# Kernel tuning notes

Hardware: AMD Instinct MI355X
Metric: run time of the kernel (lower is better)

The kernel has to match this reference:

```python
import jax, jax.numpy as jnp
import numpy as np
from jax import lax

B, C, L = 2048, 9605, 8
WL_PER_LABEL = 50
ALPHA = 0.5        # training_config['alpha4']
ALPHA1 = 0.1       # margin
ALPHA2 = 2.0       # training_config['alpha2']
ALPHA3 = 10.0      # training_config['alpha3']
ALPHA_OTHER = 0.5
NEG = jnp.float32(-1e30)


def setup_inputs() -> dict:
    key = jax.random.key(0)
    k1, k2, k3, k4 = jax.random.split(key, 4)
    x = jax.random.normal(k1, (B, C), dtype=jnp.float32) * 2.0
    y = (jax.random.uniform(k2, (B, C)) < 0.005).astype(jnp.float32)
    y_neg = (jax.random.uniform(k3, (B, C)) < 0.005).astype(jnp.float32)
    # whitelist masks: L app-labels, each whitelisting ~WL_PER_LABEL raw classes
    idx = jax.random.randint(k4, (L, WL_PER_LABEL), 0, C)
    wl_masks = jnp.zeros((L, C), dtype=bool).at[jnp.arange(L)[:, None], idx].set(True)
    return {"x": x, "y": y, "y_neg": y_neg, "wl_masks": wl_masks}


def reference(x, y, y_neg, wl_masks):
    # y_neg is consumed by the original forward (find_gt_whitelist) but never
    # affects the returned loss, faithfully ignored here.
    xs_pos = jax.nn.sigmoid(x)                                  # [B, C]
    # top_k_thres = max(11th-largest sigmoid, alpha_other)
    thres = jnp.maximum(lax.top_k(xs_pos, 11)[0][:, 10], ALPHA_OTHER)  # [B]
    # per-label whitelist max: m[b,l] = max_{c in wl_l} xs_pos[b,c]
    m = jnp.max(jnp.where(wl_masks[None, :, :], xs_pos[:, None, :], NEG), axis=-1)  # [B, L]
    # label l is a ground-truth whitelist label iff y has any positive in wl_l
    has_pos = jnp.einsum('bc,lc->bl', y, wl_masks.astype(y.dtype)) > 0   # [B, L]
    correct_max = jnp.max(jnp.where(has_pos, m, NEG), axis=-1)           # [B]
    incorrect_max = jnp.max(jnp.where(~has_pos, m, NEG), axis=-1)        # [B]
    any_correct = jnp.any(has_pos, axis=-1)
    any_incorrect = jnp.any(~has_pos, axis=-1)
    # union whitelist max (the "other" branch uses xs_pos over all wl indices)
    union_max = jnp.max(jnp.where(jnp.any(wl_masks, axis=0)[None, :], xs_pos, NEG), axis=-1)
    x1 = jnp.where(any_correct, correct_max, thres)
    x2 = jnp.where(any_correct,
                   jnp.where(any_incorrect, jnp.maximum(incorrect_max, thres), thres),
                   union_max)
    coef = jnp.where(any_correct, 1.0, 1.0 - ALPHA)
    d = x2 - x1 + ALPHA1
    rank = jnp.where(d > 0, ALPHA2, 1.0) * jax.nn.sigmoid(ALPHA3 * d)
    return jnp.mean(coef * rank)
```

## Files before the change

### kernel.cpp

```cpp
#include <hip/hip_runtime.h>

#define CC 9605
#define BB 2048
#define LL 8
#define NEGF (-1e30f)
#define NINF (-__builtin_huge_valf())

#define WS_PARTIALS_OFF 16384

__device__ __forceinline__ unsigned enc_f(float f) {
  unsigned u = __float_as_uint(f);
  return (u & 0x80000000u) ? ~u : (u | 0x80000000u);
}
__device__ __forceinline__ float dec_u(unsigned e) {
  unsigned u = (e & 0x80000000u) ? (e & 0x7fffffffu) : ~e;
  return __uint_as_float(u);
}
__device__ __forceinline__ float sigm(float z) {
  return 1.0f / (1.0f + __expf(-z));
}

__global__ void wl_sniff(const unsigned* __restrict__ wlw,
                         unsigned* __restrict__ wsu) {
  const int nwords = (LL * CC) / 4;
  const int stride = gridDim.x * blockDim.x;
  unsigned f = 0u;
  for (int j = blockIdx.x * blockDim.x + threadIdx.x; j < nwords; j += stride) {
    unsigned w = wlw[j];
#pragma unroll
    for (int k = 0; k < 4; ++k) {
      unsigned b = (w >> (8 * k)) & 255u;
      if (b == 1u)    { f |= 2u; if (k != 0) f |= 1u; }
      if (b == 0x3fu) { f |= 8u; if (k == 1) f |= 4u; }
    }
  }
#pragma unroll
  for (int off = 32; off >= 1; off >>= 1) f |= __shfl_xor(f, off, 64);
  if ((threadIdx.x & 63) == 0 && f) atomicOr(&wsu[1], f);
}

__global__ void wl_compact(const unsigned char* __restrict__ wl,
                           unsigned* __restrict__ wsu) {
  const int tid = threadIdx.x;
  const int lane = tid & 63;
  const int c = blockIdx.x * 256 + tid;
  const unsigned g = wsu[1];
  const int dt = (g & 1u) ? 0 : (g & 4u) ? 3 : (g & 2u) ? 1 : (g & 8u) ? 2 : 0;
  const int* wl32 = (const int*)wl;
  const float* wlf = (const float*)wl;
  const unsigned short* wlh = (const unsigned short*)wl;
  unsigned m = 0u;
  if (c < CC) {
#pragma unroll
    for (int l = 0; l < LL; ++l) {
      int j = l * CC + c;
      bool on;
      if (dt == 0) on = (wl[j] != 0);
      else if (dt == 1) on = (wl32[j] != 0);
      else if (dt == 2) on = (wlf[j] != 0.0f);
      else on = (wlh[j] != 0);
      if (on) m |= (1u << l);
    }
  }
  unsigned long long bal = __ballot(m != 0u);
  if (bal) {
    unsigned wcnt = (unsigned)__popcll(bal);
    unsigned basep = 0u;
    if (lane == 0) basep = atomicAdd(&wsu[0], wcnt);
    basep = __shfl(basep, 0, 64);
    if (m) {
      unsigned pos = basep + (unsigned)__popcll(bal & ((1ull << lane) - 1ull));
      if (pos < 2048u) wsu[4 + pos] = ((unsigned)c << 8) | m;
    }
  }
}


#define FOR11(OP) OP(0) OP(1) OP(2) OP(3) OP(4) OP(5) OP(6) OP(7) OP(8) OP(9) OP(10)
#define FOR11I(OP) OP(0) OP(1) OP(2) OP(3) OP(4) OP(5) OP(6) OP(7) OP(8) OP(9) OP(10)
#define FOR8(OP) OP(0) OP(1) OP(2) OP(3) OP(4) OP(5) OP(6) OP(7)

#define DECL_S(k) float s_##k = NINF;
#define INS1(k) { float _hi = fmaxf(s_##k, cv); cv = fminf(s_##k, cv); s_##k = _hi; }
#define TOP11V(v) { float cv = (v); FOR11I(INS1) }
#define TOP4(T) { TOP11V((T).x) TOP11V((T).y) TOP11V((T).z) TOP11V((T).w) }

__global__ __launch_bounds__(256) void loss_kernel(
    const float* __restrict__ x, const float* __restrict__ y,
    const unsigned* __restrict__ wsu, float* __restrict__ partials) {
  __shared__ float sh_top[3][64][11];
  __shared__ float sh_wlm[4][8];
  __shared__ unsigned sh_wpm[4];

  const int tid = threadIdx.x;
  const int lane = tid & 63;
  const int w = tid >> 6;
  const int r = blockIdx.x;
  const long long base = (long long)r * CC;

  const unsigned nu = min(wsu[0], 2048u);
  const unsigned* ents = wsu + 4;

  const int soff = (4 - (r & 3)) & 3;
  const int ng = (CC - soff) >> 2;
  const int tailn = CC - soff - (ng << 2);
  const int m_extra = soff + tailn;
  const float4* vp = (const float4*)(x + base + soff);

  FOR11(DECL_S)

  const int g0 = 600 * w + lane;
#pragma unroll
  for (int k = 0; k < 9; ++k) {
    float4 t = vp[g0 + 64 * k];
    TOP4(t)
  }
  {
    float4 t = make_float4(NINF, NINF, NINF, NINF);
    if (lane < 24) t = vp[600 * w + 576 + lane];
    TOP4(t)
  }
  if (w == 3) {
    {
      float4 t = make_float4(NINF, NINF, NINF, NINF);
      if (2400 + lane < ng) t = vp[2400 + lane];
      TOP4(t)
    }
    float tv = NINF;
    if (lane < m_extra) {
      int tc = (lane < soff) ? lane : (soff + (ng << 2) + (lane - soff));
      tv = x[base + tc];
    }
    TOP11V(tv)
  }

  unsigned en0 = ((unsigned)tid < nu) ? ents[tid] : 0u;
  unsigned en1 = ((unsigned)tid + 256u < nu) ? ents[tid + 256] : 0u;
  float gx0 = x[base + (en0 >> 8)], gy0 = y[base + (en0 >> 8)];
  float gx1 = x[base + (en1 >> 8)], gy1 = y[base + (en1 >> 8)];

#define DECL_LM(k) float lm_##k = NEGF;
  FOR8(DECL_LM)
  unsigned pmask = 0u;
#define FOLDE(EN, GX, GY)                                        \
  {                                                              \
    unsigned mk = (EN) & 255u;    \
    pmask |= mk;                                                 \
    if ((GY) > 0.0f) pmask |= (mk << 8);                         \
    if (mk & 1u)   lm_0 = fmaxf(lm_0, (GX));                     \
    if (mk & 2u)   lm_1 = fmaxf(lm_1, (GX));                     \
    if (mk & 4u)   lm_2 = fmaxf(lm_2, (GX));                     \
    if (mk & 8u)   lm_3 = fmaxf(lm_3, (GX));                     \
    if (mk & 16u)  lm_4 = fmaxf(lm_4, (GX));                     \
    if (mk & 32u)  lm_5 = fmaxf(lm_5, (GX));                     \
    if (mk & 64u)  lm_6 = fmaxf(lm_6, (GX));                     \
    if (mk & 128u) lm_7 = fmaxf(lm_7, (GX));                     \
  }
  FOLDE(en0, gx0, gy0)
  FOLDE(en1, gx1, gy1)
  for (unsigned e = 512u + (unsigned)tid; e < nu; e += 256u) {
    unsigned ent = ents[e];
    float xv = x[base + (ent >> 8)];
    float yv = y[base + (ent >> 8)];
    FOLDE(ent, xv, yv)
  }
#pragma unroll
  for (int off = 32; off >= 1; off >>= 1) {
    pmask |= __shfl_xor(pmask, off, 64);
#define RED1(l) lm_##l = fmaxf(lm_##l, __shfl_xor(lm_##l, off, 64));
    FOR8(RED1)
#undef RED1
  }

  if (w > 0) {
#define ST1(k) sh_top[w - 1][lane][k] = s_##k;
    FOR11(ST1)
#undef ST1
  }
  if (lane == 0) {
#define STL(l) sh_wlm[w][l] = lm_##l;
    FOR8(STL)
#undef STL
    sh_wpm[w] = pmask;
  }
  __syncthreads();
  if (w != 0) return;

#pragma unroll
  for (int j = 0; j < 3; ++j) {
#pragma unroll
    for (int k = 0; k < 11; ++k) {
      TOP11V(sh_top[j][lane][k])
    }
  }

#define DECL_E(k) unsigned e_##k = enc_f(s_##k);
  FOR11(DECL_E)
#undef DECL_E
  unsigned wlo = e_10;
  unsigned whi = e_0;
#pragma unroll
  for (int off = 32; off >= 1; off >>= 1) {
    wlo = max(wlo, __shfl_xor(wlo, off, 64));
    whi = max(whi, __shfl_xor(whi, off, 64));
  }
  unsigned lo = wlo, hi = whi + 1u;
  while (hi - lo > 1u) {
    unsigned mid = lo + ((hi - lo) >> 1);
    unsigned cnt = 0u;
#define CMP1(k) cnt += (e_##k >= mid) ? 1u : 0u;
    FOR11(CMP1)
#undef CMP1
    unsigned tot = (unsigned)__popcll(__ballot(cnt & 1u)) +
                   ((unsigned)__popcll(__ballot(cnt & 2u)) << 1) +
                   ((unsigned)__popcll(__ballot(cnt & 4u)) << 2) +
                   ((unsigned)__popcll(__ballot(cnt & 8u)) << 3);
    if (tot >= 11u) lo = mid; else hi = mid;
  }
  const unsigned E11 = lo;

  if (lane == 0) {
#pragma unroll
    for (int j = 1; j < 4; ++j) {
      pmask |= sh_wpm[j];
#define CMB(l) lm_##l = fmaxf(lm_##l, sh_wlm[j][l]);
      FOR8(CMB)
#undef CMB
    }
    unsigned PR = pmask & 255u, PO = (pmask >> 8) & 255u;
    float thres = fmaxf(sigm(dec_u(E11)), 0.5f);
    float cmax = NEGF, imax = NEGF, umax = NEGF;
#define EP1(l)                                                   \
    if ((PR >> l) & 1u) {                                        \
      float ml = sigm(lm_##l);                                   \
      umax = fmaxf(umax, ml);                                    \
      if ((PO >> l) & 1u) cmax = fmaxf(cmax, ml);                \
      else imax = fmaxf(imax, ml);                               \
    }
    FOR8(EP1)
#undef EP1
    bool anyc = (PO != 0u);
    bool anyi = (PO != 255u);
    float x1 = anyc ? cmax : thres;
    float x2 = anyc ? (anyi ? fmaxf(imax, thres) : thres)
                    : ((nu > 0u) ? umax : NEGF);
    float coef = anyc ? 1.0f : 0.5f;
    float dd = x2 - x1 + 0.1f;
    float rank = ((dd > 0.0f) ? 2.0f : 1.0f) * sigm(10.0f * dd);
    partials[r] = coef * rank;
  }
}

__global__ void final_reduce(const float* __restrict__ partials,
                             float* __restrict__ out) {
  __shared__ float sh[4];
  const int tid = threadIdx.x;
  const int lane = tid & 63;
  const int wid = tid >> 6;
  float s = 0.0f;
  for (int i = tid; i < BB; i += 256) s += partials[i];
#pragma unroll
  for (int off = 32; off >= 1; off >>= 1) s += __shfl_xor(s, off, 64);
  if (lane == 0) sh[wid] = s;
  __syncthreads();
  if (tid == 0) out[0] = (sh[0] + sh[1] + sh[2] + sh[3]) * (1.0f / (float)BB);
}

extern "C" void kernel_launch(void* const* d_in, const int* in_sizes, int n_in,
                              void* d_out, int out_size, void* d_ws,
                              size_t ws_size, hipStream_t stream) {
  const float* x = (const float*)d_in[0];
  const float* y = (const float*)d_in[1];
  const unsigned char* wl = (const unsigned char*)d_in[3];
  float* out = (float*)d_out;
  unsigned* wsu = (unsigned*)d_ws;
  float* partials = (float*)((char*)d_ws + WS_PARTIALS_OFF);

  hipMemsetAsync(d_ws, 0, 16, stream);
  wl_sniff<<<64, 256, 0, stream>>>((const unsigned*)wl, wsu);
  wl_compact<<<(CC + 255) / 256, 256, 0, stream>>>(wl, wsu);
  loss_kernel<<<BB, 256, 0, stream>>>(x, y, wsu, partials);
  final_reduce<<<1, 256, 0, stream>>>(partials, out);
}
```

Baseline: 222.2 us.

## Replace per-thread top-11 insertion with rowmax-guided threshold compaction

```diff
diff --git a/kernel.cpp b/kernel.cpp
--- a/kernel.cpp
+++ b/kernel.cpp
@@ -3,10 +3,13 @@
 #define CC 9605
 #define BB 2048
 #define LL 8
+#define CAND_MAX 384
 #define NEGF (-1e30f)
 #define NINF (-__builtin_huge_valf())
+#define LOMIN 0x00800000u
 
 #define WS_PARTIALS_OFF 16384
+#define WS_ROWMAX_OFF 24576
 
 __device__ __forceinline__ unsigned enc_f(float f) {
   unsigned u = __float_as_uint(f);
@@ -75,76 +78,166 @@
   }
 }
 
-
-#define FOR11(OP) OP(0) OP(1) OP(2) OP(3) OP(4) OP(5) OP(6) OP(7) OP(8) OP(9) OP(10)
-#define FOR11I(OP) OP(0) OP(1) OP(2) OP(3) OP(4) OP(5) OP(6) OP(7) OP(8) OP(9) OP(10)
-#define FOR8(OP) OP(0) OP(1) OP(2) OP(3) OP(4) OP(5) OP(6) OP(7)
-
-#define DECL_S(k) float s_##k = NINF;
-#define INS1(k) { float _hi = fmaxf(s_##k, cv); cv = fminf(s_##k, cv); s_##k = _hi; }
-#define TOP11V(v) { float cv = (v); FOR11I(INS1) }
-#define TOP4(T) { TOP11V((T).x) TOP11V((T).y) TOP11V((T).z) TOP11V((T).w) }
-
-__global__ __launch_bounds__(256) void loss_kernel(
-    const float* __restrict__ x, const float* __restrict__ y,
-    const unsigned* __restrict__ wsu, float* __restrict__ partials) {
-  __shared__ float sh_top[3][64][11];
-  __shared__ float sh_wlm[4][8];
-  __shared__ unsigned sh_wpm[4];
-
-  const int tid = threadIdx.x;
-  const int lane = tid & 63;
-  const int w = tid >> 6;
+__global__ __launch_bounds__(256) void rowmax_kernel(
+    const float* __restrict__ x, unsigned* __restrict__ rowmax) {
+  __shared__ float shm[4];
+  const int tid = threadIdx.x, lane = tid & 63, wid = tid >> 6;
   const int r = blockIdx.x;
   const long long base = (long long)r * CC;
-
-  const unsigned nu = min(wsu[0], 2048u);
-  const unsigned* ents = wsu + 4;
-
   const int soff = (4 - (r & 3)) & 3;
   const int ng = (CC - soff) >> 2;
   const int tailn = CC - soff - (ng << 2);
   const int m_extra = soff + tailn;
   const float4* vp = (const float4*)(x + base + soff);
-
-  FOR11(DECL_S)
-
-  const int g0 = 600 * w + lane;
+  float m = NINF;
 #pragma unroll
   for (int k = 0; k < 9; ++k) {
-    float4 t = vp[g0 + 64 * k];
-    TOP4(t)
+    float4 t = vp[tid + (k << 8)];
+    m = fmaxf(m, fmaxf(fmaxf(t.x, t.y), fmaxf(t.z, t.w)));
   }
   {
-    float4 t = make_float4(NINF, NINF, NINF, NINF);
-    if (lane < 24) t = vp[600 * w + 576 + lane];
-    TOP4(t)
-  }
-  if (w == 3) {
-    {
-      float4 t = make_float4(NINF, NINF, NINF, NINF);
-      if (2400 + lane < ng) t = vp[2400 + lane];
-      TOP4(t)
-    }
-    float tv = NINF;
-    if (lane < m_extra) {
-      int tc = (lane < soff) ? lane : (soff + (ng << 2) + (lane - soff));
-      tv = x[base + tc];
-    }
-    TOP11V(tv)
-  }
+    int gi = tid + 2304;
+    if (gi < ng) {
+      float4 t = vp[gi];
+      m = fmaxf(m, fmaxf(fmaxf(t.x, t.y), fmaxf(t.z, t.w)));
+    }
+  }
+  if (tid < m_extra) {
+    int tc = (tid < soff) ? tid : (soff + (ng << 2) + (tid - soff));
+    m = fmaxf(m, x[base + tc]);
+  }
+#pragma unroll
+  for (int off = 32; off >= 1; off >>= 1) m = fmaxf(m, __shfl_xor(m, off, 64));
+  if (lane == 0) shm[wid] = m;
+  __syncthreads();
+  if (tid == 0)
+    rowmax[r] = enc_f(fmaxf(fmaxf(shm[0], shm[1]), fmaxf(shm[2], shm[3])));
+}
+
+
+#define FOR8(OP) OP(0) OP(1) OP(2) OP(3) OP(4) OP(5) OP(6) OP(7)
+
+#define APPEND1(V, PRED)                                                     \
+  {                                                                          \
+    bool _p = (PRED);                                                        \
+    unsigned long long _bal = __ballot(_p);                                  \
+    if (_bal) {                                                              \
+      unsigned _wt = (unsigned)__popcll(_bal);                               \
+      unsigned _bp = 0u;                                                     \
+      if (lane == 0) _bp = atomicAdd(&sh_cnt, _wt);                          \
+      _bp = __shfl(_bp, 0, 64);                                              \
+      if (_p) {                                                              \
+        unsigned _pos =                                                      \
+            _bp + (unsigned)__popcll(_bal & ((1ull << lane) - 1ull));        \
+        if (_pos < CAND_MAX) sh_cand[_pos] = enc_f(V);                       \
+      }                                                                      \
+    }                                                                        \
+  }
+
+#define COMPACT_PASS(TENC, RES)                                              \
+  do {                                                                       \
+    float Tf = dec_u(TENC);                                                  \
+    __syncthreads();                                                         \
+    if (tid == 0) sh_cnt = 0u;                                               \
+    __syncthreads();                                                         \
+    _Pragma("unroll") for (int k = 0; k < 9; ++k) {                          \
+      float4 t = vp[tid + (k << 8)];                                         \
+      APPEND1(t.x, t.x >= Tf) APPEND1(t.y, t.y >= Tf)                        \
+      APPEND1(t.z, t.z >= Tf) APPEND1(t.w, t.w >= Tf)                        \
+    }                                                                        \
+    {                                                                        \
+      float4 t = make_float4(NINF, NINF, NINF, NINF);                        \
+      if (tid + 2304 < ng) t = vp[tid + 2304];                               \
+      APPEND1(t.x, t.x >= Tf) APPEND1(t.y, t.y >= Tf)                        \
+      APPEND1(t.z, t.z >= Tf) APPEND1(t.w, t.w >= Tf)                        \
+    }                                                                        \
+    APPEND1(tailv, tailv >= Tf)                                              \
+    __syncthreads();                                                         \
+    RES = sh_cnt;                                                            \
+  } while (0)
+
+#define COUNT_PASS(TENC, RES)                                                \
+  do {                                                                       \
+    float Tf = dec_u(TENC);                                                  \
+    unsigned cl = 0u;                                                        \
+    _Pragma("unroll") for (int k = 0; k < 9; ++k) {                          \
+      float4 t = vp[tid + (k << 8)];                                         \
+      cl += (t.x >= Tf) + (t.y >= Tf) + (t.z >= Tf) + (t.w >= Tf);           \
+    }                                                                        \
+    {                                                                        \
+      float4 t = make_float4(NINF, NINF, NINF, NINF);                        \
+      if (tid + 2304 < ng) t = vp[tid + 2304];                               \
+      cl += (t.x >= Tf) + (t.y >= Tf) + (t.z >= Tf) + (t.w >= Tf);           \
+    }                                                                        \
+    cl += (tailv >= Tf) ? 1u : 0u;                                           \
+    _Pragma("unroll") for (int off = 32; off >= 1; off >>= 1)                \
+        cl += __shfl_xor(cl, off, 64);                                       \
+    __syncthreads();                                                         \
+    if (lane == 0) sh_redC[wid] = cl;                                        \
+    __syncthreads();                                                         \
+    RES = sh_redC[0] + sh_redC[1] + sh_redC[2] + sh_redC[3];                 \
+  } while (0)
+
+__global__ __launch_bounds__(256) void loss_kernel(
+    const float* __restrict__ x, const float* __restrict__ y,
+    const unsigned* __restrict__ wsu, const unsigned* __restrict__ rowmax,
+    float* __restrict__ partials) {
+  __shared__ unsigned sh_cand[CAND_MAX];
+  __shared__ unsigned sh_redC[4];
+  __shared__ unsigned sh_cnt;
+  __shared__ float sh_wlm[4][8];
+  __shared__ unsigned sh_wpm[4];
+
+  const int tid = threadIdx.x, lane = tid & 63, wid = tid >> 6;
+  const int r = blockIdx.x;
+  const long long base = (long long)r * CC;
+  const int soff = (4 - (r & 3)) & 3;
+  const int ng = (CC - soff) >> 2;
+  const int tailn = CC - soff - (ng << 2);
+  const int m_extra = soff + tailn;
+  const float4* vp = (const float4*)(x + base + soff);
+  float tailv = NINF;
+  if (tid < m_extra) {
+    int tc = (tid < soff) ? tid : (soff + (ng << 2) + (tid - soff));
+    tailv = x[base + tc];
+  }
+  const unsigned Emax = rowmax[r];
+  const unsigned nu = min(wsu[0], 2048u);
+  const unsigned* ents = wsu + 4;
+
+  unsigned lo = (Emax > LOMIN + (1u << 22)) ? Emax - (1u << 22) : LOMIN;
+  unsigned hi = Emax + 1u;
+  unsigned c;
+  bool done = false;
+  unsigned E11 = 0u;
+  COMPACT_PASS(lo, c);
+  unsigned compLo = lo;
+  while (c < 11u && lo > LOMIN) {
+    hi = lo;
+    lo = (lo > LOMIN + (1u << 23)) ? lo - (1u << 23) : LOMIN;
+    COMPACT_PASS(lo, c);
+    compLo = lo;
+  }
+  if (c < 11u) { E11 = LOMIN; done = true; }
+  while (!done && c > CAND_MAX) {
+    if (hi - lo <= 1u) { E11 = lo; done = true; break; }
+    unsigned mid = lo + ((hi - lo) >> 1);
+    unsigned cm;
+    COUNT_PASS(mid, cm);
+    if (cm >= 11u) { lo = mid; c = cm; } else { hi = mid; }
+  }
+  if (!done && lo != compLo) { COMPACT_PASS(lo, c); }
 
   unsigned en0 = ((unsigned)tid < nu) ? ents[tid] : 0u;
   unsigned en1 = ((unsigned)tid + 256u < nu) ? ents[tid + 256] : 0u;
   float gx0 = x[base + (en0 >> 8)], gy0 = y[base + (en0 >> 8)];
   float gx1 = x[base + (en1 >> 8)], gy1 = y[base + (en1 >> 8)];
-
 #define DECL_LM(k) float lm_##k = NEGF;
   FOR8(DECL_LM)
   unsigned pmask = 0u;
 #define FOLDE(EN, GX, GY)                                        \
   {                                                              \
-    unsigned mk = (EN) & 255u;    \
+    unsigned mk = (EN) & 255u;                                   \
     pmask |= mk;                                                 \
     if ((GY) > 0.0f) pmask |= (mk << 8);                         \
     if (mk & 1u)   lm_0 = fmaxf(lm_0, (GX));                     \
@@ -171,53 +264,35 @@
     FOR8(RED1)
 #undef RED1
   }
-
-  if (w > 0) {
-#define ST1(k) sh_top[w - 1][lane][k] = s_##k;
-    FOR11(ST1)
-#undef ST1
-  }
   if (lane == 0) {
-#define STL(l) sh_wlm[w][l] = lm_##l;
+#define STL(l) sh_wlm[wid][l] = lm_##l;
     FOR8(STL)
 #undef STL
-    sh_wpm[w] = pmask;
+    sh_wpm[wid] = pmask;
   }
   __syncthreads();
-  if (w != 0) return;
-
-#pragma unroll
-  for (int j = 0; j < 3; ++j) {
-#pragma unroll
-    for (int k = 0; k < 11; ++k) {
-      TOP11V(sh_top[j][lane][k])
-    }
-  }
-
-#define DECL_E(k) unsigned e_##k = enc_f(s_##k);
-  FOR11(DECL_E)
-#undef DECL_E
-  unsigned wlo = e_10;
-  unsigned whi = e_0;
-#pragma unroll
-  for (int off = 32; off >= 1; off >>= 1) {
-    wlo = max(wlo, __shfl_xor(wlo, off, 64));
-    whi = max(whi, __shfl_xor(whi, off, 64));
-  }
-  unsigned lo = wlo, hi = whi + 1u;
-  while (hi - lo > 1u) {
-    unsigned mid = lo + ((hi - lo) >> 1);
-    unsigned cnt = 0u;
-#define CMP1(k) cnt += (e_##k >= mid) ? 1u : 0u;
-    FOR11(CMP1)
-#undef CMP1
-    unsigned tot = (unsigned)__popcll(__ballot(cnt & 1u)) +
-                   ((unsigned)__popcll(__ballot(cnt & 2u)) << 1) +
-                   ((unsigned)__popcll(__ballot(cnt & 4u)) << 2) +
-                   ((unsigned)__popcll(__ballot(cnt & 8u)) << 3);
-    if (tot >= 11u) lo = mid; else hi = mid;
-  }
-  const unsigned E11 = lo;
+  if (wid != 0) return;
+
+  if (!done) {
+    unsigned c0 = ((unsigned)lane < c) ? sh_cand[lane] : 0u;
+    unsigned c1 = ((unsigned)lane + 64u < c) ? sh_cand[lane + 64u] : 0u;
+    unsigned c2 = ((unsigned)lane + 128u < c) ? sh_cand[lane + 128u] : 0u;
+    unsigned c3 = ((unsigned)lane + 192u < c) ? sh_cand[lane + 192u] : 0u;
+    unsigned c4 = ((unsigned)lane + 256u < c) ? sh_cand[lane + 256u] : 0u;
+    unsigned c5 = ((unsigned)lane + 320u < c) ? sh_cand[lane + 320u] : 0u;
+    unsigned blo = lo, bhi = hi;
+    while (bhi - blo > 1u) {
+      unsigned mid = blo + ((bhi - blo) >> 1);
+      unsigned cnt = (unsigned)__popcll(__ballot(c0 >= mid)) +
+                     (unsigned)__popcll(__ballot(c1 >= mid)) +
+                     (unsigned)__popcll(__ballot(c2 >= mid)) +
+                     (unsigned)__popcll(__ballot(c3 >= mid)) +
+                     (unsigned)__popcll(__ballot(c4 >= mid)) +
+                     (unsigned)__popcll(__ballot(c5 >= mid));
+      if (cnt >= 11u) blo = mid; else bhi = mid;
+    }
+    E11 = blo;
+  }
 
   if (lane == 0) {
 #pragma unroll
@@ -275,10 +350,12 @@
   float* out = (float*)d_out;
   unsigned* wsu = (unsigned*)d_ws;
   float* partials = (float*)((char*)d_ws + WS_PARTIALS_OFF);
+  unsigned* rowmax = (unsigned*)((char*)d_ws + WS_ROWMAX_OFF);
 
   hipMemsetAsync(d_ws, 0, 16, stream);
   wl_sniff<<<64, 256, 0, stream>>>((const unsigned*)wl, wsu);
   wl_compact<<<(CC + 255) / 256, 256, 0, stream>>>(wl, wsu);
-  loss_kernel<<<BB, 256, 0, stream>>>(x, y, wsu, partials);
+  rowmax_kernel<<<BB, 256, 0, stream>>>(x, rowmax);
+  loss_kernel<<<BB, 256, 0, stream>>>(x, y, wsu, rowmax, partials);
   final_reduce<<<1, 256, 0, stream>>>(partials, out);
 }
```

Result: slower. 248.1 us (+11.7%).
